# Kernel tuning notes

Hardware: AMD Instinct MI355X
Metric: run time of the kernel (lower is better)

Reference implementation:

```python
import jax, jax.numpy as jnp
import numpy as np
from jax import lax

D_MODEL = 192
D_STATE = 128
D_CONV = 3
EXPAND = 2
HEADDIM = 64
NGROUPS = 1
CHUNK = 256
K = 4  # scan directions
D_INNER = EXPAND * D_MODEL          # 384
D_SSM = D_INNER                     # 384
NHEADS = D_SSM // HEADDIM           # 6
HH = K * NHEADS                     # 24 heads total (dir-major)
CONV_CH = D_SSM + 2 * NGROUPS * D_STATE + NHEADS  # 646 (conv applied to x,B,C,dt channels)
D_IN_PROJ = 2 * D_INNER + 2 * NGROUPS * D_STATE + NHEADS  # 1030
BSZ, HIMG, WIMG = 4, 64, 64


def setup_inputs() -> dict:
    key = jax.random.key(0)
    ks = jax.random.split(key, 8)
    u = jax.random.normal(ks[0], (BSZ, HIMG, WIMG, D_MODEL), jnp.float32)
    W_in = jax.random.normal(ks[1], (D_MODEL, D_IN_PROJ), jnp.float32) * 0.02
    conv_w = jax.random.normal(ks[2], (CONV_CH, 1, D_CONV, D_CONV), jnp.float32) * 0.1
    conv_b = jnp.zeros((CONV_CH,), jnp.float32)
    # dt_bias init per source: inverse-softplus of dt ~ LogUniform(1e-3, 1e-1), tiled over 4 dirs
    dt = jnp.exp(jax.random.uniform(ks[3], (NHEADS,)) * (np.log(0.1) - np.log(0.001)) + np.log(0.001))
    dt = jnp.maximum(dt, 1e-4)
    inv_dt = dt + jnp.log(-jnp.expm1(-dt))
    dt_bias = jnp.tile(inv_dt[None, :], (K, 1))  # (4, nheads)
    A = jax.random.uniform(ks[4], (NHEADS,), minval=1.0, maxval=16.0)
    A_logs = jnp.tile(jnp.log(A), (K,))          # (24,)
    Ds = jnp.ones((HH,), jnp.float32)
    norm_w = jnp.ones((D_SSM,), jnp.float32)
    W_out = jax.random.normal(ks[5], (D_INNER, D_MODEL), jnp.float32) * 0.02
    return dict(u=u, W_in=W_in, conv_w=conv_w, conv_b=conv_b, dt_bias=dt_bias,
                A_logs=A_logs, Ds=Ds, norm_w=norm_w, W_out=W_out)


def _ssd(x, dt, A, Bm, Cm, chunk):
    """Chunked selective state-space scan (Mamba2 SSD).
    x: (b,L,H,P), dt: (b,L,H) (post-softplus), A: (H,) negative scalars,
    Bm/Cm: (b,L,G,N) with heads grouped G-major (H = G*hpg)."""
    b, L, H, P = x.shape
    G, N = Bm.shape[2], Bm.shape[3]
    hpg = H // G
    nc = L // chunk
    x = x.reshape(b, nc, chunk, G, hpg, P)
    dt = dt.reshape(b, nc, chunk, G, hpg)
    Bm = Bm.reshape(b, nc, chunk, G, N)
    Cm = Cm.reshape(b, nc, chunk, G, N)
    dA = dt * A.reshape(G, hpg)                 # (b,z,c,g,h), negative
    dAc = jnp.cumsum(dA, axis=2)                # within-chunk cumsum
    dAt = jnp.transpose(dAc, (0, 1, 3, 4, 2))   # (b,z,g,h,c)
    idx = jnp.arange(chunk)
    mask = idx[:, None] >= idx[None, :]         # causal within chunk
    seg = jnp.exp(jnp.where(mask, dAt[..., :, None] - dAt[..., None, :], -1e30))  # (b,z,g,h,c,s)
    CB = jnp.einsum('bzcgn,bzsgn->bzgcs', Cm, Bm)
    xdt = x * dt[..., None]                     # dt applied at source position
    y_intra = jnp.einsum('bzghcs,bzsghp->bzcghp', CB[:, :, :, None] * seg, xdt)
    decay_last = jnp.exp(dAc[:, :, -1:] - dAc)  # (b,z,c,g,h)
    states = jnp.einsum('bzcgn,bzcghp->bzghpn', Bm, xdt * decay_last[..., None])
    cd = jnp.exp(dAc[:, :, -1])                 # (b,z,g,h) whole-chunk decay

    def step(carry, inp):
        s, c = inp
        return carry * c[..., None, None] + s, carry  # emit state entering the chunk

    _, prevs = lax.scan(step, jnp.zeros_like(states[:, 0]),
                        (jnp.swapaxes(states, 0, 1), jnp.swapaxes(cd, 0, 1)))
    prev = jnp.swapaxes(prevs, 0, 1)            # (b,z,g,h,P,N)
    y_inter = jnp.einsum('bzcgn,bzghpn->bzcghp', Cm, prev) * jnp.exp(dAc)[..., None]
    return (y_intra + y_inter).reshape(b, L, H, P)


def reference(u, W_in, conv_w, conv_b, dt_bias, A_logs, Ds, norm_w, W_out):
    B, H, W, C = u.shape
    L = H * W
    zxbcdt = u @ W_in                            # (B,H,W,1030); d_mlp == 0
    z = zxbcdt[..., :D_SSM]                      # gate
    xBCdt = zxbcdt[..., D_SSM:]                  # (B,H,W,CONV_CH)
    # depthwise 3x3 conv + SiLU (NCHW)
    xb = jnp.transpose(xBCdt, (0, 3, 1, 2))
    xb = lax.conv_general_dilated(xb, conv_w, (1, 1), 'SAME',
                                  feature_group_count=CONV_CH,
                                  dimension_numbers=('NCHW', 'OIHW', 'NCHW'))
    xb = jax.nn.silu(xb + conv_b[None, :, None, None])
    # 4 scan directions: row-major, col-major, and their reverses
    d0 = xb.reshape(B, CONV_CH, L)
    d1 = jnp.transpose(xb, (0, 1, 3, 2)).reshape(B, CONV_CH, L)
    dirs = jnp.stack([d0, d1], axis=1)
    dirs = jnp.concatenate([dirs, jnp.flip(dirs, axis=-1)], axis=1)  # (B,4,CONV_CH,L)
    seq = jnp.transpose(dirs, (0, 3, 1, 2))      # (B,L,4,CONV_CH)
    xs = seq[..., :D_SSM].reshape(B, L, HH, HEADDIM)
    Bs = seq[..., D_SSM:D_SSM + D_STATE]         # (B,L,4,N), ngroups=1 -> G=4 dirs
    Cs = seq[..., D_SSM + D_STATE:D_SSM + 2 * D_STATE]
    dts = seq[..., D_SSM + 2 * D_STATE:].reshape(B, L, HH)
    dt = jax.nn.softplus(dts + dt_bias.reshape(HH))
    A = -jnp.exp(A_logs)                         # (HH,)
    y = _ssd(xs, dt, A, Bs, Cs, CHUNK) + xs * Ds[None, None, :, None]
    y = y.reshape(B, L, K, D_SSM)
    y0 = y[:, :, 0]
    y1 = y[:, :, 1]
    y2 = jnp.flip(y[:, :, 2], axis=1)
    y3 = jnp.flip(y[:, :, 3], axis=1)
    wh1 = jnp.transpose(y1.reshape(B, W, H, D_SSM), (0, 2, 1, 3)).reshape(B, L, D_SSM)
    wh3 = jnp.transpose(y3.reshape(B, W, H, D_SSM), (0, 2, 1, 3)).reshape(B, L, D_SSM)
    out = (y0 + y2 + wh1 + wh3).reshape(B, H, W, D_SSM)
    # RMSNormGated (norm_before_gate=False, group_size = d_ssm)
    g = out * jax.nn.silu(z)
    g = g * lax.rsqrt(jnp.mean(g * g, axis=-1, keepdims=True) + 1e-5) * norm_w
    return g @ W_out
```

## Files before the change

kernel.cpp:

```cpp
#include <hip/hip_runtime.h>
#include <hip/hip_fp16.h>
#include <math.h>

#define BQ 4
#define LQ 4096
#define DM 192
#define DIP 1030
#define DSSM 384
#define DST 128
#define CCH 646
#define CH640 640
#define NHD 6
#define KDIR 4
#define NCH 16
#define CLEN 256
#define UH_ELEMS (16384 * 192)
#define WT_ELEMS (1152 * 192)

using half8 = __attribute__((ext_vector_type(8))) _Float16;
using half4 = __attribute__((ext_vector_type(4))) _Float16;
using f32x4 = __attribute__((ext_vector_type(4))) float;

#define XWI(pp, ss) ((pp) * 72 + ((((ss) >> 3) ^ ((pp) >> 3)) << 3) + ((ss) & 7))
#define XW2(n, ss) ((n) * 72 + (((((ss) >> 3) ^ ((n) >> 3)) & 7) << 3) + ((ss) & 7))

__device__ __forceinline__ int pixof(int k, int t) {
  switch (k) {
    case 0: return t;
    case 1: return ((t & 63) << 6) | (t >> 6);
    case 2: return 4095 - t;
    default: { int tp = 4095 - t; return ((tp & 63) << 6) | (tp >> 6); }
  }
}

__device__ __forceinline__ float softplusf(float x) {
  return (x > 20.f) ? x : log1pf(expf(x));
}
__device__ __forceinline__ float siluf(float x) {
  return x / (1.f + __expf(-x));
}

__global__ void k_cvt(const float* __restrict__ u, const float* __restrict__ W,
                      _Float16* __restrict__ uh, _Float16* __restrict__ whT) {
  int idx = blockIdx.x * 256 + threadIdx.x;
  if (idx < UH_ELEMS) uh[idx] = (_Float16)u[idx];
  int widx = idx - UH_ELEMS;
  if (widx >= 0 && widx < WT_ELEMS) {
    int n = widx / 192, kk = widx - n * 192;
    whT[widx] = (n < DIP) ? (_Float16)W[(size_t)kk * DIP + n] : (_Float16)0.f;
  }
}

__global__ __launch_bounds__(256) void k_inproj(
    const _Float16* __restrict__ uh, const _Float16* __restrict__ whT,
    __half* __restrict__ zh, __half* __restrict__ xbch, float* __restrict__ xdt32) {
  __shared__ __align__(16) _Float16 sA[128 * 72];
  __shared__ __align__(16) _Float16 sB[128 * 72];
  int nt = blockIdx.x, mt = blockIdx.y;
  int m0 = mt * 128, n0 = nt * 128;
  int t = threadIdx.x, lane = t & 63, w = t >> 6;
  int acol = lane & 15, koff = (lane >> 4) * 8;
  int wr = w >> 1, wc = w & 1;
  f32x4 zz = {0.f, 0.f, 0.f, 0.f};
  f32x4 acc[4][4];
#pragma unroll
  for (int fr = 0; fr < 4; ++fr)
#pragma unroll
    for (int fc = 0; fc < 4; ++fc) acc[fr][fc] = zz;
  for (int kk = 0; kk < 3; ++kk) {
    if (kk) __syncthreads();
#pragma unroll
    for (int i = 0; i < 4; ++i) {
      int task = t + i * 256;
      int row = task >> 3, oct = task & 7;
      *(half8*)&sA[row * 72 + oct * 8] =
          *(const half8*)&uh[(size_t)(m0 + row) * 192 + kk * 64 + oct * 8];
      *(half8*)&sB[row * 72 + oct * 8] =
          *(const half8*)&whT[(size_t)(n0 + row) * 192 + kk * 64 + oct * 8];
    }
    __syncthreads();
#pragma unroll
    for (int ks = 0; ks < 2; ++ks) {
      half8 af[4], bf[4];
#pragma unroll
      for (int f = 0; f < 4; ++f) {
        af[f] = *(const half8*)&sA[(wr * 64 + f * 16 + acol) * 72 + ks * 32 + koff];
        bf[f] = *(const half8*)&sB[(wc * 64 + f * 16 + acol) * 72 + ks * 32 + koff];
      }
#pragma unroll
      for (int fr = 0; fr < 4; ++fr)
#pragma unroll
        for (int fc = 0; fc < 4; ++fc)
          acc[fr][fc] = __builtin_amdgcn_mfma_f32_16x16x32_f16(af[fr], bf[fc], acc[fr][fc], 0, 0, 0);
    }
  }
  int rb = (lane >> 4) * 4;
#pragma unroll
  for (int fr = 0; fr < 4; ++fr) {
#pragma unroll
    for (int fc = 0; fc < 4; ++fc) {
      int n = n0 + wc * 64 + fc * 16 + acol;
#pragma unroll
      for (int r = 0; r < 4; ++r) {
        int m = m0 + wr * 64 + fr * 16 + rb + r;
        float v = acc[fr][fc][r];
        if (n < DSSM) zh[(size_t)m * DSSM + n] = (__half)v;
        else if (n < 1024) xbch[(size_t)m * CH640 + (n - DSSM)] = (__half)v;
        else if (n < DIP) xdt32[(size_t)m * NHD + (n - 1024)] = v;
      }
    }
  }
}

__global__ void k_conv(const __half* __restrict__ xbch, const float* __restrict__ xdt,
                       const float* __restrict__ cw, const float* __restrict__ cb,
                       __half* __restrict__ convh, float* __restrict__ dtraw) {
  int pid = blockIdx.x;
  int b = pid >> 12, p = pid & 4095;
  int y = p >> 6, x = p & 63;
  int t = threadIdx.x;
  const __half2* baseh2 = (const __half2*)(xbch + (size_t)b * LQ * CH640);
  __half2* outh2 = (__half2*)(convh + (size_t)pid * CH640);
  for (int pc = t; pc < 320; pc += 256) {
    int c0 = pc * 2;
    float s0 = 0.f, s1 = 0.f;
#pragma unroll
    for (int ky = 0; ky < 3; ++ky) {
      int yy = y + ky - 1;
      if (yy < 0 || yy > 63) continue;
#pragma unroll
      for (int kx = 0; kx < 3; ++kx) {
        int xx = x + kx - 1;
        if (xx < 0 || xx > 63) continue;
        __half2 v = baseh2[(size_t)(yy * 64 + xx) * 320 + pc];
        int wi = ky * 3 + kx;
        s0 += (float)v.x * cw[c0 * 9 + wi];
        s1 += (float)v.y * cw[(c0 + 1) * 9 + wi];
      }
    }
    __half2 o;
    o.x = (__half)siluf(s0 + cb[c0]);
    o.y = (__half)siluf(s1 + cb[c0 + 1]);
    outh2[pc] = o;
  }
  if (t < NHD) {
    const float* based = xdt + (size_t)b * LQ * NHD;
    float s = 0.f;
#pragma unroll
    for (int ky = 0; ky < 3; ++ky) {
      int yy = y + ky - 1;
      if (yy < 0 || yy > 63) continue;
#pragma unroll
      for (int kx = 0; kx < 3; ++kx) {
        int xx = x + kx - 1;
        if (xx < 0 || xx > 63) continue;
        s += based[(size_t)(yy * 64 + xx) * NHD + t] * cw[(CH640 + t) * 9 + ky * 3 + kx];
      }
    }
    dtraw[(size_t)pid * NHD + t] = siluf(s + cb[CH640 + t]);
  }
}

__global__ void k_prep(const float* __restrict__ dtraw, const float* __restrict__ dt_bias,
                       const float* __restrict__ A_logs,
                       float* __restrict__ dtb, float* __restrict__ dacb) {
  __shared__ float sb[CLEN];
  int z = blockIdx.x, k = blockIdx.y, b = blockIdx.z;
  int s = threadIdx.x;
  int pixel = pixof(k, z * CLEN + s);
  const float* row = dtraw + ((size_t)(b * LQ + pixel)) * NHD;
  float raw[NHD];
#pragma unroll
  for (int h = 0; h < NHD; ++h) raw[h] = row[h];
  size_t base = (((size_t)(b * KDIR + k) * NCH + z) * NHD) * CLEN;
  for (int h = 0; h < NHD; ++h) {
    float dtv = softplusf(raw[h] + dt_bias[k * NHD + h]);
    float dA = dtv * (-expf(A_logs[k * NHD + h]));
    sb[s] = dA;
    __syncthreads();
    for (int off = 1; off < CLEN; off <<= 1) {
      float v = (s >= off) ? sb[s - off] : 0.f;
      __syncthreads();
      sb[s] += v;
      __syncthreads();
    }
    dtb[base + (size_t)h * CLEN + s] = dtv;
    dacb[base + (size_t)h * CLEN + s] = sb[s];
    __syncthreads();
  }
}

__global__ __launch_bounds__(256, 4) void k_cb(const _Float16* __restrict__ convh,
                                               _Float16* __restrict__ cbuf) {
  __shared__ __align__(16) char smem[34816];
  _Float16* sCt = (_Float16*)smem;
  _Float16* sBt = (_Float16*)(smem + 17408);
  int pi = blockIdx.x, z = blockIdx.y, bk = blockIdx.z;
  int b = bk >> 2, kd = bk & 3;
  int SI = 0;
  while ((SI + 1) * (SI + 2) / 2 <= pi) ++SI;
  int SJ = pi - SI * (SI + 1) / 2;
  int t = threadIdx.x, lane = t & 63, w = t >> 6;
  int acol = lane & 15, koff = (lane >> 4) * 8;
  int R = w * 16, arow = R + acol, rbase = R + (lane >> 4) * 4;
  const _Float16* convb = convh + (size_t)b * LQ * CH640;
  for (int i = 0; i < 4; ++i) {
    int c = t + i * 256;
    int row = c >> 4, seg = c & 15;
    int pc = pixof(kd, z * CLEN + SI * 64 + row);
    *(half8*)&sCt[row * 136 + seg * 8] =
        *(const half8*)&convb[(size_t)pc * CH640 + (DSSM + DST) + seg * 8];
    int pbx = pixof(kd, z * CLEN + SJ * 64 + row);
    *(half8*)&sBt[row * 136 + seg * 8] =
        *(const half8*)&convb[(size_t)pbx * CH640 + DSSM + seg * 8];
  }
  __syncthreads();
  f32x4 zz = {0.f, 0.f, 0.f, 0.f};
  f32x4 acc[4] = {zz, zz, zz, zz};
  for (int ks = 0; ks < 4; ++ks) {
    half8 a = *(const half8*)&sCt[arow * 136 + ks * 32 + koff];
#pragma unroll
    for (int cg = 0; cg < 4; ++cg) {
      half8 bf = *(const half8*)&sBt[(cg * 16 + acol) * 136 + ks * 32 + koff];
      acc[cg] = __builtin_amdgcn_mfma_f32_16x16x32_f16(a, bf, acc[cg], 0, 0, 0);
    }
  }
  size_t base = ((size_t)(bk * NCH + z) * 10 + pi) * 4096;
#pragma unroll
  for (int cg = 0; cg < 4; ++cg)
#pragma unroll
    for (int r = 0; r < 4; ++r)
      cbuf[base + (size_t)(rbase + r) * 64 + cg * 16 + acol] = (_Float16)acc[cg][r];
}

__global__ void k_diag(const _Float16* __restrict__ cbuf, const float* __restrict__ dacb,
                       _Float16* __restrict__ dbuf) {
  __shared__ float sd[64];
  int hs = blockIdx.x;
  int si = hs / 6, h = hs % 6;
  int z = blockIdx.y, bk = blockIdx.z;
  int t = threadIdx.x;
  if (t < 64) sd[t] = dacb[(((size_t)bk * NCH + z) * NHD + h) * CLEN + si * 64 + t];
  __syncthreads();
  size_t cb = ((size_t)(bk * NCH + z) * 10 + si * (si + 1) / 2 + si) * 4096;
  size_t db = (((size_t)(bk * NCH + z) * 4 + si) * NHD + h) * 4096;
#pragma unroll
  for (int i = 0; i < 16; ++i) {
    int e = t + i * 256;
    int sl = e >> 6, ss = e & 63;
    _Float16 v = (_Float16)0.f;
    if (ss <= sl) v = (_Float16)((float)cbuf[cb + e] * __expf(sd[sl] - sd[ss]));
    dbuf[db + e] = v;
  }
}

__global__ __launch_bounds__(256, 4) void k_states(
    const _Float16* __restrict__ convh, const float* __restrict__ dtb,
    const float* __restrict__ dacb, _Float16* __restrict__ statesT) {
  __shared__ __align__(16) _Float16 sA[64 * 72];
  __shared__ __align__(16) _Float16 sB2[128 * 72];
  __shared__ float sFac[CLEN];
  int h = blockIdx.x, z = blockIdx.y, bk = blockIdx.z;
  int b = bk >> 2, kd = bk & 3;
  int t = threadIdx.x, lane = t & 63, w = t >> 6;
  int acol = lane & 15, koct = lane >> 4;
  size_t dbase = (((size_t)bk * NCH + z) * NHD + h) * CLEN;
  {
    float dac_last = dacb[dbase + CLEN - 1];
    sFac[t] = dtb[dbase + t] * __expf(dac_last - dacb[dbase + t]);
  }
  __syncthreads();
  const _Float16* convb = convh + (size_t)b * LQ * CH640;
  f32x4 zz = {0.f, 0.f, 0.f, 0.f};
  f32x4 acc[8] = {zz, zz, zz, zz, zz, zz, zz, zz};
  for (int st = 0; st < 4; ++st) {
    if (st) __syncthreads();
#pragma unroll
    for (int i = 0; i < 2; ++i) {
      int c = t + i * 256;
      int ss = c >> 3, pp0 = (c & 7) * 8;
      int sg = st * 64 + ss;
      int px = pixof(kd, z * CLEN + sg);
      half8 xv = *(const half8*)&convb[(size_t)px * CH640 + h * 64 + pp0];
      float f = sFac[sg];
#pragma unroll
      for (int u = 0; u < 8; ++u) sA[XWI(pp0 + u, ss)] = (_Float16)((float)xv[u] * f);
    }
#pragma unroll
    for (int i = 0; i < 4; ++i) {
      int c = t + i * 256;
      int ss = c >> 4, n0 = (c & 15) * 8;
      int sg = st * 64 + ss;
      int px = pixof(kd, z * CLEN + sg);
      half8 bv = *(const half8*)&convb[(size_t)px * CH640 + DSSM + n0];
#pragma unroll
      for (int u = 0; u < 8; ++u) sB2[XW2(n0 + u, ss)] = bv[u];
    }
    __syncthreads();
#pragma unroll
    for (int ks = 0; ks < 2; ++ks) {
      int kso = ks * 4 + koct;
      int arow = w * 16 + acol;
      half8 a = *(const half8*)&sA[arow * 72 + ((kso ^ (arow >> 3)) << 3)];
#pragma unroll
      for (int nf = 0; nf < 8; ++nf) {
        int col = nf * 16 + acol;
        half8 bf = *(const half8*)&sB2[col * 72 + (((kso ^ (col >> 3)) & 7) << 3)];
        acc[nf] = __builtin_amdgcn_mfma_f32_16x16x32_f16(a, bf, acc[nf], 0, 0, 0);
      }
    }
  }
  size_t sbase = (((size_t)bk * NCH + z) * NHD + h) * (128 * 64);
  int rbase = koct * 4;
#pragma unroll
  for (int nf = 0; nf < 8; ++nf) {
    int col = nf * 16 + acol;
#pragma unroll
    for (int r = 0; r < 4; ++r)
      statesT[sbase + (size_t)(w * 16 + rbase + r) * 128 + col] = (_Float16)acc[nf][r];
  }
}

__global__ void k_scan(_Float16* __restrict__ states, const float* __restrict__ dacb) {
  int h = blockIdx.x, k = blockIdx.y, b = blockIdx.z;
  int bk = b * KDIR + k;
  int t = threadIdx.x;
  float carry[32];
#pragma unroll
  for (int j = 0; j < 32; ++j) carry[j] = 0.f;
  for (int z = 0; z < NCH; ++z) {
    float cd = __expf(dacb[(((size_t)bk * NCH + z) * NHD + h) * CLEN + (CLEN - 1)]);
    size_t sbase = (((size_t)bk * NCH + z) * NHD + h) * (128 * 64);
#pragma unroll
    for (int j = 0; j < 32; ++j) {
      size_t idx = sbase + (size_t)j * 256 + t;
      float sv = (float)states[idx];
      states[idx] = (_Float16)carry[j];
      carry[j] = carry[j] * cd + sv;
    }
  }
}

__global__ __launch_bounds__(256, 4) void k_y(
    const _Float16* __restrict__ convh, const float* __restrict__ dtb,
    const float* __restrict__ dacb, const _Float16* __restrict__ cbuf,
    const _Float16* __restrict__ prevT, const _Float16* __restrict__ dbuf,
    const float* __restrict__ Ds, _Float16* __restrict__ ybuf) {
  __shared__ __align__(16) _Float16 sXW[64 * 72];
  __shared__ float sdt[CLEN], sdac[CLEN], sFac[CLEN];
  __shared__ float sExpD[64], sRs[64];

  int wg = blockIdx.x;
  int xid = (wg & 7) * 768 + (wg >> 3);
  int grp = xid / 24, i24 = xid % 24;
  int h = i24 >> 2, si_t = i24 & 3;
  int bk = grp >> 4, z = grp & 15;
  int b = bk >> 2, kd = bk & 3;
  int t = threadIdx.x, lane = t & 63, w = t >> 6;
  int acol = lane & 15, koff = (lane >> 4) * 8;
  int R = w * 16, arow = R + acol, rbase = R + (lane >> 4) * 4;

  size_t dbase = (((size_t)bk * NCH + z) * NHD + h) * CLEN;
  sdt[t] = dtb[dbase + t];
  sdac[t] = dacb[dbase + t];
  __syncthreads();
  float ref = sdac[si_t * 64];
  sFac[t] = __expf(ref - sdac[t]);
  if (t < 64) {
    float d = sdac[si_t * 64 + t];
    sExpD[t] = __expf(d);
    sRs[t] = __expf(d - ref);
  }
  const _Float16* convb = convh + (size_t)b * LQ * CH640;
  const _Float16* pbp = prevT + (((size_t)bk * NCH + z) * NHD + h) * (128 * 64);
  f32x4 zz = {0.f, 0.f, 0.f, 0.f};
  f32x4 accE[4] = {zz, zz, zz, zz};
  f32x4 accI[4] = {zz, zz, zz, zz};
  int pxa = pixof(kd, z * CLEN + si_t * 64 + arow);
#pragma unroll
  for (int ks = 0; ks < 4; ++ks) {
    half8 a = *(const half8*)&convb[(size_t)pxa * CH640 + (DSSM + DST) + ks * 32 + koff];
#pragma unroll
    for (int cg = 0; cg < 4; ++cg) {
      half8 bf = *(const half8*)&pbp[(size_t)(cg * 16 + acol) * 128 + ks * 32 + koff];
      accE[cg] = __builtin_amdgcn_mfma_f32_16x16x32_f16(a, bf, accE[cg], 0, 0, 0);
    }
  }
  __syncthreads();
  for (int SJ = 0; SJ < si_t; ++SJ) {
#pragma unroll
    for (int i = 0; i < 2; ++i) {
      int c = t + i * 256;
      int ss = c >> 3, pp0 = (c & 7) * 8;
      int sg = SJ * 64 + ss;
      int px = pixof(kd, z * CLEN + sg);
      half8 xv = *(const half8*)&convb[(size_t)px * CH640 + h * 64 + pp0];
      float f = sdt[sg] * sFac[sg];
#pragma unroll
      for (int u = 0; u < 8; ++u)
        sXW[XWI(pp0 + u, ss)] = (_Float16)((float)xv[u] * f);
    }
    __syncthreads();
    size_t cbase = ((size_t)(bk * NCH + z) * 10 + si_t * (si_t + 1) / 2 + SJ) * 4096;
#pragma unroll
    for (int ks = 0; ks < 2; ++ks) {
      half8 a = *(const half8*)&cbuf[cbase + (size_t)arow * 64 + ks * 32 + koff];
      int kso = ks * 4 + (lane >> 4);
#pragma unroll
      for (int cg = 0; cg < 4; ++cg) {
        int col = cg * 16 + acol;
        half8 bf = *(const half8*)&sXW[col * 72 + ((kso ^ (col >> 3)) << 3)];
        accI[cg] = __builtin_amdgcn_mfma_f32_16x16x32_f16(a, bf, accI[cg], 0, 0, 0);
      }
    }
    __syncthreads();
  }
  {
    float rsv[4];
#pragma unroll
    for (int r = 0; r < 4; ++r) rsv[r] = sRs[rbase + r];
#pragma unroll
    for (int cg = 0; cg < 4; ++cg)
#pragma unroll
      for (int r = 0; r < 4; ++r) accI[cg][r] *= rsv[r];
  }
  {
#pragma unroll
    for (int i = 0; i < 2; ++i) {
      int c = t + i * 256;
      int ss = c >> 3, pp0 = (c & 7) * 8;
      int sg = si_t * 64 + ss;
      int px = pixof(kd, z * CLEN + sg);
      half8 xv = *(const half8*)&convb[(size_t)px * CH640 + h * 64 + pp0];
      float f = sdt[sg];
#pragma unroll
      for (int u = 0; u < 8; ++u)
        sXW[XWI(pp0 + u, ss)] = (_Float16)((float)xv[u] * f);
    }
    __syncthreads();
    size_t db = (((size_t)(bk * NCH + z) * 4 + si_t) * NHD + h) * 4096;
#pragma unroll
    for (int ks = 0; ks < 2; ++ks) {
      half8 a = *(const half8*)&dbuf[db + (size_t)arow * 64 + ks * 32 + koff];
      int kso = ks * 4 + (lane >> 4);
#pragma unroll
      for (int cg = 0; cg < 4; ++cg) {
        int col = cg * 16 + acol;
        half8 bf = *(const half8*)&sXW[col * 72 + ((kso ^ (col >> 3)) << 3)];
        accI[cg] = __builtin_amdgcn_mfma_f32_16x16x32_f16(a, bf, accI[cg], 0, 0, 0);
      }
    }
  }
  float dsv = Ds[kd * NHD + h];
  float eD[4];
#pragma unroll
  for (int r = 0; r < 4; ++r) eD[r] = sExpD[rbase + r];
#pragma unroll
  for (int cg = 0; cg < 4; ++cg) {
    int col = cg * 16 + acol;
#pragma unroll
    for (int r = 0; r < 4; ++r) {
      int row = rbase + r;
      int tg = z * CLEN + si_t * 64 + row;
      int px = pixof(kd, tg);
      float xv = (float)convb[(size_t)px * CH640 + h * 64 + col];
      float yv = accI[cg][r] + eD[r] * accE[cg][r] + dsv * xv;
      ybuf[((size_t)bk * LQ + tg) * DSSM + h * 64 + col] = (_Float16)yv;
    }
  }
}

__global__ void k_final(const __half* __restrict__ yb, const __half* __restrict__ zh,
                        const float* __restrict__ norm_w, const float* __restrict__ Wout,
                        float* __restrict__ out) {
  __shared__ float sg[8 * DSSM];
  __shared__ float srstd[8];
  int m0 = blockIdx.x * 8;
  int t = threadIdx.x;
  for (int rr = 0; rr < 8; ++rr) {
    int m = m0 + rr, b = m >> 12, px = m & 4095;
    int tr = ((px & 63) << 6) | (px >> 6);
    int t0 = px, t1 = tr, t2 = 4095 - px, t3 = 4095 - tr;
    size_t b4 = (size_t)b * 4;
    for (int c = t; c < DSSM; c += 256) {
      float yv = (float)yb[((b4 + 0) * LQ + t0) * DSSM + c] +
                 (float)yb[((b4 + 1) * LQ + t1) * DSSM + c] +
                 (float)yb[((b4 + 2) * LQ + t2) * DSSM + c] +
                 (float)yb[((b4 + 3) * LQ + t3) * DSSM + c];
      float zv = (float)zh[(size_t)m * DSSM + c];
      sg[rr * DSSM + c] = yv * (zv / (1.f + __expf(-zv)));
    }
  }
  __syncthreads();
  {
    int r = t >> 5, j = t & 31;
    float s = 0.f;
    for (int c = j; c < DSSM; c += 32) { float g = sg[r * DSSM + c]; s += g * g; }
    s += __shfl_xor(s, 16, 32);
    s += __shfl_xor(s, 8, 32);
    s += __shfl_xor(s, 4, 32);
    s += __shfl_xor(s, 2, 32);
    s += __shfl_xor(s, 1, 32);
    if (j == 0) srstd[r] = rsqrtf(s / (float)DSSM + 1e-5f);
  }
  __syncthreads();
  for (int rr = 0; rr < 8; ++rr)
    for (int c = t; c < DSSM; c += 256) sg[rr * DSSM + c] *= srstd[rr] * norm_w[c];
  __syncthreads();
  if (t < DM) {
    float a[8];
#pragma unroll
    for (int rr = 0; rr < 8; ++rr) a[rr] = 0.f;
    for (int c = 0; c < DSSM; ++c) {
      float wv = Wout[(size_t)c * DM + t];
#pragma unroll
      for (int rr = 0; rr < 8; ++rr) a[rr] += sg[rr * DSSM + c] * wv;
    }
#pragma unroll
    for (int rr = 0; rr < 8; ++rr) out[(size_t)(m0 + rr) * DM + t] = a[rr];
  }
}

extern "C" void kernel_launch(void* const* d_in, const int* in_sizes, int n_in,
                              void* d_out, int out_size, void* d_ws, size_t ws_size,
                              hipStream_t stream) {
  const float* u = (const float*)d_in[0];
  const float* W_in = (const float*)d_in[1];
  const float* conv_w = (const float*)d_in[2];
  const float* conv_b = (const float*)d_in[3];
  const float* dt_bias = (const float*)d_in[4];
  const float* A_logs = (const float*)d_in[5];
  const float* Ds = (const float*)d_in[6];
  const float* norm_w = (const float*)d_in[7];
  const float* W_out = (const float*)d_in[8];
  float* out = (float*)d_out;

  float* ws = (float*)d_ws;
  size_t off = 0;
  __half* zh = (__half*)(ws + off); off += (size_t)BQ * LQ * DSSM / 2;
  float* scratch = ws + off; off += 1683456;
  _Float16* uh = (_Float16*)scratch;
  _Float16* whT = uh + UH_ELEMS;
  float* dtraw = scratch;
  float* dtb = scratch + 98304;
  float* dacb = scratch + 98304 + 393216;
  __half* xbch = (__half*)(ws + off); off += (size_t)BQ * LQ * CH640 / 2;
  float* xdt32 = ws + off; off += (size_t)BQ * LQ * NHD;
  __half* convh = (__half*)(ws + off); off += (size_t)BQ * LQ * CH640 / 2;
  _Float16* statesT = (_Float16*)(ws + off); off += (size_t)BQ * KDIR * NCH * NHD * 128 * 64 / 2;
  __half* ybuf = (__half*)(ws + off); off += (size_t)BQ * KDIR * LQ * DSSM / 2;
  _Float16* dbuf = (_Float16*)(ws + off); off += (size_t)BQ * KDIR * NCH * 4 * NHD * 4096 / 2;
  _Float16* cbuf = (_Float16*)xbch;

  k_cvt<<<(UH_ELEMS + WT_ELEMS) / 256, 256, 0, stream>>>(u, W_in, uh, whT);
  k_inproj<<<dim3(9, 128), 256, 0, stream>>>(uh, whT, zh, xbch, xdt32);
  k_conv<<<BQ * LQ, 256, 0, stream>>>(xbch, xdt32, conv_w, conv_b, convh, dtraw);
  k_prep<<<dim3(NCH, KDIR, BQ), 256, 0, stream>>>(dtraw, dt_bias, A_logs, dtb, dacb);
  k_cb<<<dim3(10, NCH, BQ * KDIR), 256, 0, stream>>>((const _Float16*)convh, cbuf);
  k_diag<<<dim3(24, NCH, BQ * KDIR), 256, 0, stream>>>(cbuf, dacb, dbuf);
  k_states<<<dim3(NHD, NCH, BQ * KDIR), 256, 0, stream>>>((const _Float16*)convh, dtb, dacb, statesT);
  k_scan<<<dim3(NHD, KDIR, BQ), 256, 0, stream>>>(statesT, dacb);
  k_y<<<KDIR * NHD * 4 * NCH * BQ, 256, 0, stream>>>((const _Float16*)convh, dtb, dacb,
                                                     (const _Float16*)cbuf, statesT, dbuf, Ds,
                                                     (_Float16*)ybuf);
  k_final<<<BQ * LQ / 8, 256, 0, stream>>>(ybuf, zh, norm_w, W_out, out);
}
```

Baseline: 495.9 us.

## Rewrite final norm and output projection with MFMA and vectorized loads

The final kernel now gives each row to 8 threads. Those threads load y and z with half8 vector loads, do the RMS reduction with lane shuffles, and write the normalized fp16 rows to shared memory. The output projection then runs on fp16 MFMA 16x16x32 against a transposed fp16 copy of W_out, prepared in the conversion kernel. This replaces the scalar fp32 FMA loop and the extra barriers. k_y's launch bounds also change from 4 to 8 waves per SIMD target, which may force register spills. The output GEMM loses some precision by running in fp16.

After: 445.9 us. 1.11x faster.

```diff
diff --git a/kernel.cpp b/kernel.cpp
--- a/kernel.cpp
+++ b/kernel.cpp
@@ -16,6 +16,7 @@
 #define CLEN 256
 #define UH_ELEMS (16384 * 192)
 #define WT_ELEMS (1152 * 192)
+#define WO_ELEMS (192 * 384)
 
 using half8 = __attribute__((ext_vector_type(8))) _Float16;
 using half4 = __attribute__((ext_vector_type(4))) _Float16;
@@ -41,13 +42,20 @@
 }
 
 __global__ void k_cvt(const float* __restrict__ u, const float* __restrict__ W,
-                      _Float16* __restrict__ uh, _Float16* __restrict__ whT) {
+                      const float* __restrict__ Wout,
+                      _Float16* __restrict__ uh, _Float16* __restrict__ whT,
+                      _Float16* __restrict__ woT) {
   int idx = blockIdx.x * 256 + threadIdx.x;
   if (idx < UH_ELEMS) uh[idx] = (_Float16)u[idx];
   int widx = idx - UH_ELEMS;
   if (widx >= 0 && widx < WT_ELEMS) {
     int n = widx / 192, kk = widx - n * 192;
     whT[widx] = (n < DIP) ? (_Float16)W[(size_t)kk * DIP + n] : (_Float16)0.f;
+  }
+  int wo = idx - UH_ELEMS - WT_ELEMS;
+  if (wo >= 0 && wo < WO_ELEMS) {
+    int n = wo / 384, kk = wo - n * 384;
+    woT[wo] = (_Float16)Wout[(size_t)kk * DM + n];
   }
 }
 
@@ -341,7 +349,7 @@
   }
 }
 
-__global__ __launch_bounds__(256, 4) void k_y(
+__global__ __launch_bounds__(256, 8) void k_y(
     const _Float16* __restrict__ convh, const float* __restrict__ dtb,
     const float* __restrict__ dacb, const _Float16* __restrict__ cbuf,
     const _Float16* __restrict__ prevT, const _Float16* __restrict__ dbuf,
@@ -470,54 +478,71 @@
   }
 }
 
-__global__ void k_final(const __half* __restrict__ yb, const __half* __restrict__ zh,
-                        const float* __restrict__ norm_w, const float* __restrict__ Wout,
-                        float* __restrict__ out) {
-  __shared__ float sg[8 * DSSM];
-  __shared__ float srstd[8];
-  int m0 = blockIdx.x * 8;
+__global__ __launch_bounds__(256) void k_final(
+    const _Float16* __restrict__ yb, const _Float16* __restrict__ zh,
+    const float* __restrict__ norm_w, const _Float16* __restrict__ woT,
+    float* __restrict__ out) {
+  __shared__ __align__(16) _Float16 sG[32 * 392];
+  int m0 = blockIdx.x * 32;
   int t = threadIdx.x;
-  for (int rr = 0; rr < 8; ++rr) {
-    int m = m0 + rr, b = m >> 12, px = m & 4095;
-    int tr = ((px & 63) << 6) | (px >> 6);
-    int t0 = px, t1 = tr, t2 = 4095 - px, t3 = 4095 - tr;
-    size_t b4 = (size_t)b * 4;
-    for (int c = t; c < DSSM; c += 256) {
-      float yv = (float)yb[((b4 + 0) * LQ + t0) * DSSM + c] +
-                 (float)yb[((b4 + 1) * LQ + t1) * DSSM + c] +
-                 (float)yb[((b4 + 2) * LQ + t2) * DSSM + c] +
-                 (float)yb[((b4 + 3) * LQ + t3) * DSSM + c];
-      float zv = (float)zh[(size_t)m * DSSM + c];
-      sg[rr * DSSM + c] = yv * (zv / (1.f + __expf(-zv)));
-    }
+  int row = t >> 3, q = t & 7;
+  int m = m0 + row, b = m >> 12, px = m & 4095;
+  int tr = ((px & 63) << 6) | (px >> 6);
+  int t0 = px, t1 = tr, t2 = 4095 - px, t3 = 4095 - tr;
+  size_t b4 = (size_t)b * 4;
+  float gbuf[48];
+  float sumsq = 0.f;
+#pragma unroll
+  for (int i = 0; i < 6; ++i) {
+    int c0 = q * 48 + i * 8;
+    half8 y0 = *(const half8*)&yb[((b4 + 0) * LQ + t0) * DSSM + c0];
+    half8 y1 = *(const half8*)&yb[((b4 + 1) * LQ + t1) * DSSM + c0];
+    half8 y2 = *(const half8*)&yb[((b4 + 2) * LQ + t2) * DSSM + c0];
+    half8 y3 = *(const half8*)&yb[((b4 + 3) * LQ + t3) * DSSM + c0];
+    half8 zv8 = *(const half8*)&zh[(size_t)m * DSSM + c0];
+#pragma unroll
+    for (int u = 0; u < 8; ++u) {
+      float zv = (float)zv8[u];
+      float g = ((float)y0[u] + (float)y1[u] + (float)y2[u] + (float)y3[u]) *
+                (zv / (1.f + __expf(-zv)));
+      gbuf[i * 8 + u] = g;
+      sumsq += g * g;
+    }
+  }
+  sumsq += __shfl_xor(sumsq, 1);
+  sumsq += __shfl_xor(sumsq, 2);
+  sumsq += __shfl_xor(sumsq, 4);
+  float rstd = rsqrtf(sumsq / (float)DSSM + 1e-5f);
+#pragma unroll
+  for (int i = 0; i < 6; ++i) {
+    int c0 = q * 48 + i * 8;
+    half8 gv;
+#pragma unroll
+    for (int u = 0; u < 8; ++u)
+      gv[u] = (_Float16)(gbuf[i * 8 + u] * rstd * norm_w[c0 + u]);
+    *(half8*)&sG[row * 392 + c0] = gv;
   }
   __syncthreads();
-  {
-    int r = t >> 5, j = t & 31;
-    float s = 0.f;
-    for (int c = j; c < DSSM; c += 32) { float g = sg[r * DSSM + c]; s += g * g; }
-    s += __shfl_xor(s, 16, 32);
-    s += __shfl_xor(s, 8, 32);
-    s += __shfl_xor(s, 4, 32);
-    s += __shfl_xor(s, 2, 32);
-    s += __shfl_xor(s, 1, 32);
-    if (j == 0) srstd[r] = rsqrtf(s / (float)DSSM + 1e-5f);
-  }
-  __syncthreads();
-  for (int rr = 0; rr < 8; ++rr)
-    for (int c = t; c < DSSM; c += 256) sg[rr * DSSM + c] *= srstd[rr] * norm_w[c];
-  __syncthreads();
-  if (t < DM) {
-    float a[8];
-#pragma unroll
-    for (int rr = 0; rr < 8; ++rr) a[rr] = 0.f;
-    for (int c = 0; c < DSSM; ++c) {
-      float wv = Wout[(size_t)c * DM + t];
-#pragma unroll
-      for (int rr = 0; rr < 8; ++rr) a[rr] += sg[rr * DSSM + c] * wv;
-    }
-#pragma unroll
-    for (int rr = 0; rr < 8; ++rr) out[(size_t)(m0 + rr) * DM + t] = a[rr];
+  int lane = t & 63, w = t >> 6;
+  int acol = lane & 15, koff = (lane >> 4) * 8;
+  int rt = (w & 1) * 16, cb0 = (w >> 1) * 96;
+  f32x4 zz = {0.f, 0.f, 0.f, 0.f};
+  f32x4 acc[6] = {zz, zz, zz, zz, zz, zz};
+  for (int ks = 0; ks < 12; ++ks) {
+    half8 a = *(const half8*)&sG[(rt + acol) * 392 + ks * 32 + koff];
+#pragma unroll
+    for (int nf = 0; nf < 6; ++nf) {
+      half8 bf = *(const half8*)&woT[(size_t)(cb0 + nf * 16 + acol) * 384 + ks * 32 + koff];
+      acc[nf] = __builtin_amdgcn_mfma_f32_16x16x32_f16(a, bf, acc[nf], 0, 0, 0);
+    }
+  }
+  int rb = (lane >> 4) * 4;
+#pragma unroll
+  for (int nf = 0; nf < 6; ++nf) {
+    int n = cb0 + nf * 16 + acol;
+#pragma unroll
+    for (int r = 0; r < 4; ++r)
+      out[(size_t)(m0 + rt + rb + r) * DM + n] = acc[nf][r];
   }
 }
 
@@ -550,9 +575,10 @@
   _Float16* statesT = (_Float16*)(ws + off); off += (size_t)BQ * KDIR * NCH * NHD * 128 * 64 / 2;
   __half* ybuf = (__half*)(ws + off); off += (size_t)BQ * KDIR * LQ * DSSM / 2;
   _Float16* dbuf = (_Float16*)(ws + off); off += (size_t)BQ * KDIR * NCH * 4 * NHD * 4096 / 2;
+  _Float16* woT = (_Float16*)(ws + off); off += WO_ELEMS / 2;
   _Float16* cbuf = (_Float16*)xbch;
 
-  k_cvt<<<(UH_ELEMS + WT_ELEMS) / 256, 256, 0, stream>>>(u, W_in, uh, whT);
+  k_cvt<<<(UH_ELEMS + WT_ELEMS + WO_ELEMS + 255) / 256, 256, 0, stream>>>(u, W_in, W_out, uh, whT, woT);
   k_inproj<<<dim3(9, 128), 256, 0, stream>>>(uh, whT, zh, xbch, xdt32);
   k_conv<<<BQ * LQ, 256, 0, stream>>>(xbch, xdt32, conv_w, conv_b, convh, dtraw);
   k_prep<<<dim3(NCH, KDIR, BQ), 256, 0, stream>>>(dtraw, dt_bias, A_logs, dtb, dacb);
@@ -563,5 +589,6 @@
   k_y<<<KDIR * NHD * 4 * NCH * BQ, 256, 0, stream>>>((const _Float16*)convh, dtb, dacb,
                                                      (const _Float16*)cbuf, statesT, dbuf, Ds,
                                                      (_Float16*)ybuf);
-  k_final<<<BQ * LQ / 8, 256, 0, stream>>>(ybuf, zh, norm_w, W_out, out);
-}
+  k_final<<<BQ * LQ / 32, 256, 0, stream>>>((const _Float16*)ybuf, (const _Float16*)zh,
+                                            norm_w, woT, out);
+}
```
